# Kernel optimization log

Measured on AMD Instinct MI355X. Metric: run time of the kernel, lower is better.

## Reference

```python
import jax, jax.numpy as jnp
import numpy as np

B, N1, N2, D, H = 2, 1024, 1024, 2048, 16
DH = D // H  # 128


def _rope_tables(S, d):
    inv = 1.0 / (10000.0 ** (np.arange(0, d, 2, dtype=np.float32) / d))
    ang = np.outer(np.arange(S, dtype=np.float32), inv)  # [S, d/2]
    cos = np.repeat(np.cos(ang), 2, axis=-1).astype(np.float32)  # [S, d] interleaved pairs
    sin = np.repeat(np.sin(ang), 2, axis=-1).astype(np.float32)
    return jnp.asarray(cos), jnp.asarray(sin)


def setup_inputs() -> dict:
    key = jax.random.key(0)
    ks = jax.random.split(key, 24)
    sc = 0.02
    cos1, sin1 = _rope_tables(N1, DH)
    cos2, sin2 = _rope_tables(N2, DH)
    inp = {
        'x_1': jax.random.normal(ks[0], (B, N1, D), dtype=jnp.float32),
        'x_2': jax.random.normal(ks[1], (B, N2, D), dtype=jnp.float32),
        'cos1': cos1, 'sin1': sin1, 'cos2': cos2, 'sin2': sin2,
    }
    names = ['wq1', 'wk1', 'wv1', 'wo1', 'wq2', 'wk2', 'wv2', 'wo2']
    for i, n in enumerate(names):
        inp[n] = jax.random.normal(ks[2 + i], (D, D), dtype=jnp.float32) * sc
        inp['b' + n[1:]] = jax.random.normal(ks[10 + i], (D,), dtype=jnp.float32) * sc
    return inp


def _apply_rope(x, cos, sin):
    # x: [B, H, S, DH]; interleaved-pair rotation (use_real_unbind_dim=-1)
    xr = x.reshape(*x.shape[:-1], -1, 2)
    x_real, x_imag = xr[..., 0], xr[..., 1]
    x_rot = jnp.stack([-x_imag, x_real], axis=-1).reshape(x.shape)
    return x * cos[None, None] + x_rot * sin[None, None]


def _split_heads(t):
    b, n, _ = t.shape
    return t.reshape(b, n, H, DH).transpose(0, 2, 1, 3)  # b h n c


def reference(x_1, x_2, cos1, sin1, cos2, sin2,
              wq1, bq1, wk1, bk1, wv1, bv1, wo1, bo1,
              wq2, bq2, wk2, bk2, wv2, bv2, wo2, bo2):
    len_1 = x_1.shape[1]
    q = jnp.concatenate([x_1 @ wq1 + bq1, x_2 @ wq2 + bq2], axis=1)
    k = jnp.concatenate([x_1 @ wk1 + bk1, x_2 @ wk2 + bk2], axis=1)
    v = jnp.concatenate([x_1 @ wv1 + bv1, x_2 @ wv2 + bv2], axis=1)
    q, k, v = _split_heads(q), _split_heads(k), _split_heads(v)
    q = q * (DH ** -0.5)
    # per-position RoPE on the concatenated stream == per-stream RoPE then concat
    cos = jnp.concatenate([cos1, cos2], axis=0)
    sin = jnp.concatenate([sin1, sin2], axis=0)
    q = _apply_rope(q, cos, sin)
    k = _apply_rope(k, cos, sin)
    # joint attention over both streams (independent/cross_only flags = False)
    scores = jnp.einsum('bhqd,bhkd->bhqk', q, k)
    attn = jax.nn.softmax(scores, axis=-1)
    o = jnp.einsum('bhqk,bhkd->bhqd', attn, v)
    o = o.transpose(0, 2, 1, 3).reshape(o.shape[0], -1, H * DH)  # b n (h c)
    o1 = o[:, :len_1] @ wo1 + bo1
    o2 = o[:, len_1:] @ wo2 + bo2
    return (o1, o2)
```

## Files before the change

### kernel.cpp

```cpp
#include <hip/hip_runtime.h>
#include <hip/hip_bf16.h>

typedef __attribute__((ext_vector_type(4))) float f32x4;
typedef __attribute__((ext_vector_type(8))) short short8;
typedef __attribute__((ext_vector_type(4))) unsigned short us4;
typedef __attribute__((ext_vector_type(2))) unsigned short us2;
typedef unsigned short u16;

__device__ __forceinline__ float bf2f(u16 u) {
  unsigned int x = ((unsigned int)u) << 16;
  float f; __builtin_memcpy(&f, &x, 4); return f;
}
__device__ __forceinline__ u16 f2bf(float f) {
  __hip_bfloat16 h = __float2bfloat16(f);
  u16 u; __builtin_memcpy(&u, &h, 2); return u;
}

#define GLL16(g, l) __builtin_amdgcn_global_load_lds( \
    (const __attribute__((address_space(1))) unsigned int*)(g), \
    (__attribute__((address_space(3))) unsigned int*)(l), 16, 0, 0)

#define MFMA16x32(a, b, c) __builtin_amdgcn_mfma_f32_16x16x32_bf16(a, b, c, 0, 0, 0)


__global__ __launch_bounds__(256) void k_convert_x(const float* __restrict__ x1,
                                                   const float* __restrict__ x2,
                                                   u16* __restrict__ xc) {
  int tid = blockIdx.x * 256 + threadIdx.x;
  int e = tid * 8;
  int m = e >> 11, d = e & 2047;
  int b = m >> 11, n = m & 2047;
  const float* src = (n < 1024) ? (x1 + ((b << 10) + n) * 2048 + d)
                                : (x2 + ((b << 10) + n - 1024) * 2048 + d);
  float4 v0 = *(const float4*)src;
  float4 v1 = *(const float4*)(src + 4);
  us4 a = {f2bf(v0.x), f2bf(v0.y), f2bf(v0.z), f2bf(v0.w)};
  us4 c = {f2bf(v1.x), f2bf(v1.y), f2bf(v1.z), f2bf(v1.w)};
  *(us4*)(xc + e) = a;
  *(us4*)(xc + e + 4) = c;
}

struct W8 { const float* w[8]; };

__global__ __launch_bounds__(256) void k_wt(W8 p, u16* __restrict__ wtbase) {
  __shared__ u16 lt[64][72];
  const float* W = p.w[blockIdx.z];
  u16* Wt = wtbase + (size_t)blockIdx.z * 4194304u;
  int k0 = blockIdx.x * 64, n0 = blockIdx.y * 64;
  int t = threadIdx.x;
#pragma unroll
  for (int i = 0; i < 4; ++i) {
    int lin = t + i * 256;
    int r = lin >> 4, c4 = (lin & 15) * 4;
    float4 v = *(const float4*)&W[(k0 + r) * 2048 + n0 + c4];
    us4 u = {f2bf(v.x), f2bf(v.y), f2bf(v.z), f2bf(v.w)};
    *(us4*)&lt[r][c4] = u;
  }
  __syncthreads();
#pragma unroll
  for (int i = 0; i < 8; ++i) {
    int lin = t + i * 256;
    int rd = lin >> 5, cs = (lin & 31) * 2;
    us2 u = {lt[cs][rd], lt[cs + 1][rd]};
    *(us2*)&Wt[(n0 + rd) * 2048 + k0 + cs] = u;
  }
}

__global__ __launch_bounds__(256) void k_vt(const u16* __restrict__ V, u16* __restrict__ Vt) {
  __shared__ u16 lt[64][72];
  int b = blockIdx.z;
  int s0 = blockIdx.x * 64, d0 = blockIdx.y * 64;
  int t = threadIdx.x;
#pragma unroll
  for (int i = 0; i < 2; ++i) {
    int lin = t + i * 256;
    int r = lin >> 3, c8 = (lin & 7) * 8;
    short8 v = *(const short8*)&V[(b * 2048 + s0 + r) * 2048 + d0 + c8];
    *(short8*)&lt[r][c8] = v;
  }
  __syncthreads();
#pragma unroll
  for (int i = 0; i < 8; ++i) {
    int lin = t + i * 256;
    int rd = lin >> 5, cs = (lin & 31) * 2;
    us2 u = {lt[cs][rd], lt[cs + 1][rd]};
    *(us2*)&Vt[(b * 2048 + d0 + rd) * 2048 + s0 + cs] = u;
  }
}

__global__ __launch_bounds__(256) void k_rope(u16* __restrict__ Qb, u16* __restrict__ Kb,
                                              const float* __restrict__ cos1,
                                              const float* __restrict__ sin1,
                                              const float* __restrict__ cos2,
                                              const float* __restrict__ sin2) {
  u16* T = blockIdx.y ? Kb : Qb;
  const float scale = blockIdx.y ? 1.f : 0.08838834764831843f;
  int tid = blockIdx.x * 256 + threadIdx.x;
  int e = tid * 8;
  int m = e >> 11;
  int n = m & 2047;
  int dh0 = e & 127;
  const float* cr; const float* sr;
  if (n < 1024) { cr = cos1 + n * 128; sr = sin1 + n * 128; }
  else          { cr = cos2 + (n - 1024) * 128; sr = sin2 + (n - 1024) * 128; }
  float4 c0 = *(const float4*)(cr + dh0), c1 = *(const float4*)(cr + dh0 + 4);
  float4 s0 = *(const float4*)(sr + dh0), s1 = *(const float4*)(sr + dh0 + 4);
  short8 xv = *(short8*)(T + e);
  float x0 = bf2f((u16)xv[0]), x1 = bf2f((u16)xv[1]), x2 = bf2f((u16)xv[2]), x3 = bf2f((u16)xv[3]);
  float x4 = bf2f((u16)xv[4]), x5 = bf2f((u16)xv[5]), x6 = bf2f((u16)xv[6]), x7 = bf2f((u16)xv[7]);
  us4 o0 = { f2bf((x0 * c0.x - x1 * s0.x) * scale), f2bf((x1 * c0.x + x0 * s0.x) * scale),
             f2bf((x2 * c0.z - x3 * s0.z) * scale), f2bf((x3 * c0.z + x2 * s0.z) * scale) };
  us4 o1 = { f2bf((x4 * c1.x - x5 * s1.x) * scale), f2bf((x5 * c1.x + x4 * s1.x) * scale),
             f2bf((x6 * c1.z - x7 * s1.z) * scale), f2bf((x7 * c1.z + x6 * s1.z) * scale) };
  *(us4*)(T + e) = o0;
  *(us4*)(T + e + 4) = o1;
}

__device__ __forceinline__ void gemm256_core(const u16* __restrict__ A,
                                             const u16* __restrict__ Bt,
                                             int m0, int nb,
                                             u16* lA, u16* lB,
                                             f32x4 acc[8][4]) {
  const int t = threadIdx.x;
  const int lane = t & 63, wid = t >> 6;
  const int lq = lane & 15, lg = lane >> 4;
  const int wr = wid >> 2, wc = wid & 3;
  const int swz = (lq & 7) << 4;

  u16* lA0 = lA;  u16* lA1 = lA + 256 * 64;
  u16* lB0 = lB;  u16* lB1 = lB + 256 * 64;

  short8 af[4][2];
  short8 bf[2][2][2];

  auto stage = [&](const u16* G, int grow0, u16* lbase, int h, int kt) {
    const int k0 = (kt & 31) * 64;
#pragma unroll
    for (int j = 0; j < 2; ++j) {
      int c = j * 512 + t;
      int row = c >> 3;
      int colb = (c & 7) * 16;
      int sc = colb ^ ((row & 7) << 4);
      GLL16(G + (size_t)(grow0 + h * 128 + row) * 2048 + k0 + (sc >> 1),
            (u16*)((char*)lbase + (h * 128 + row) * 128 + colb));
    }
  };
  auto rdA = [&](const u16* lbase, int mh) {
#pragma unroll
    for (int mf = 0; mf < 4; ++mf)
#pragma unroll
      for (int kc = 0; kc < 2; ++kc) {
        int row = wr * 128 + (mh * 4 + mf) * 16 + lq;
        af[mf][kc] = *(const short8*)((const char*)lbase + row * 128 +
                                      ((kc * 64 + lg * 16) ^ swz));
      }
  };
  auto rdB = [&](const u16* lbase, int nh) {
#pragma unroll
    for (int nf = 0; nf < 2; ++nf)
#pragma unroll
      for (int kc = 0; kc < 2; ++kc) {
        int row = wc * 64 + (nh * 2 + nf) * 16 + lq;
        bf[nh][nf][kc] = *(const short8*)((const char*)lbase + row * 128 +
                                          ((kc * 64 + lg * 16) ^ swz));
      }
  };
  auto mm = [&](int mh, int nh) {
    __builtin_amdgcn_s_setprio(1);
#pragma unroll
    for (int mf = 0; mf < 4; ++mf)
#pragma unroll
      for (int nf = 0; nf < 2; ++nf)
#pragma unroll
        for (int kc = 0; kc < 2; ++kc)
          acc[mh * 4 + mf][nh * 2 + nf] =
              MFMA16x32(af[mf][kc], bf[nh][nf][kc], acc[mh * 4 + mf][nh * 2 + nf]);
    __builtin_amdgcn_s_setprio(0);
    __builtin_amdgcn_sched_barrier(0);
  };

#define LGK0() do { asm volatile("s_waitcnt lgkmcnt(0)" ::: "memory"); \
                    __builtin_amdgcn_sched_barrier(0); } while (0)
#define BAR()  __builtin_amdgcn_s_barrier()
#define VM4()  asm volatile("s_waitcnt vmcnt(4)" ::: "memory")

  stage(Bt, nb, lB0, 0, 0);
  stage(A,  m0, lA0, 0, 0);
  stage(Bt, nb, lB0, 1, 0);
  stage(A,  m0, lA0, 1, 0);
  stage(Bt, nb, lB1, 0, 1);
  stage(A,  m0, lA1, 0, 1);
  VM4();
  BAR();

#pragma unroll 1
  for (int i = 0; i < 16; ++i) {
    const int o1 = 2 * i + 1, e2 = 2 * i + 2, o3 = 2 * i + 3;
    rdA(lA0, 0); rdB(lB0, 0);
    stage(Bt, nb, lB1, 1, o1);
    BAR(); LGK0(); mm(0, 0); BAR();
    rdB(lB0, 1);
    stage(A, m0, lA1, 1, o1);
    BAR(); LGK0(); mm(0, 1); BAR();
    rdA(lA0, 1);
    stage(Bt, nb, lB0, 0, e2);
    BAR(); LGK0(); mm(1, 0); BAR();
    stage(A, m0, lA0, 0, e2);
    BAR(); LGK0(); mm(1, 1);
    VM4(); BAR();
    rdA(lA1, 0); rdB(lB1, 0);
    stage(Bt, nb, lB0, 1, e2);
    BAR(); LGK0(); mm(0, 0); BAR();
    rdB(lB1, 1);
    stage(A, m0, lA0, 1, e2);
    BAR(); LGK0(); mm(0, 1); BAR();
    rdA(lA1, 1);
    stage(Bt, nb, lB1, 0, o3);
    BAR(); LGK0(); mm(1, 0); BAR();
    stage(A, m0, lA1, 0, o3);
    BAR(); LGK0(); mm(1, 1);
    VM4(); BAR();
  }
#undef LGK0
#undef BAR
#undef VM4
}

struct QKV8P {
  const u16* wt[6];
  const float* bias[6];
  u16* out[3];
  const u16* xc;
};

__global__ __launch_bounds__(512, 2) void k_gemm_qkv(QKV8P p) {
  __shared__ __align__(16) u16 lA[2 * 256 * 64];
  __shared__ __align__(16) u16 lB[2 * 256 * 64];
  const int id = blockIdx.x;
  const int xcd = id & 7, sub = id >> 3;
  const int nt = xcd * 3 + (sub >> 4);
  const int mt = sub & 15;
  const int m0 = mt * 256;
  const int type = nt >> 3;
  const int colw = (nt & 7) * 256;
  const int strm = (mt >> 2) & 1;
  const int widx = type * 2 + strm;
  f32x4 acc[8][4];
  const f32x4 z4 = {0.f, 0.f, 0.f, 0.f};
#pragma unroll
  for (int a = 0; a < 8; ++a)
#pragma unroll
    for (int b = 0; b < 4; ++b) acc[a][b] = z4;
  gemm256_core(p.xc, p.wt[widx], m0, colw, lA, lB, acc);
  const int lane = threadIdx.x & 63, wid = threadIdx.x >> 6;
  const int lq = lane & 15, lg = lane >> 4;
  const int wr = wid >> 2, wc = wid & 3;
  u16* out = p.out[type];
  const float* bias = p.bias[widx];
#pragma unroll
  for (int nf = 0; nf < 4; ++nf) {
    int col = colw + wc * 64 + nf * 16 + lq;
    float bv = bias[col];
#pragma unroll
    for (int mf = 0; mf < 8; ++mf) {
      int row0 = m0 + wr * 128 + mf * 16 + lg * 4;
#pragma unroll
      for (int j = 0; j < 4; ++j)
        out[(size_t)(row0 + j) * 2048 + col] = f2bf(acc[mf][nf][j] + bv);
    }
  }
}

__global__ __launch_bounds__(512, 2) void k_gemm_out(const u16* __restrict__ O,
                                                     const u16* __restrict__ wt0,
                                                     const u16* __restrict__ wt1,
                                                     const float* __restrict__ b0,
                                                     const float* __restrict__ b1,
                                                     float* __restrict__ out) {
  __shared__ __align__(16) u16 lA[2 * 256 * 64];
  __shared__ __align__(16) u16 lB[2 * 256 * 64];
  const int id = blockIdx.x;
  const int nt = id & 7, mt = id >> 3;
  const int m0 = mt * 256;
  const int strm = (mt >> 2) & 1;
  f32x4 acc[8][4];
  const f32x4 z4 = {0.f, 0.f, 0.f, 0.f};
#pragma unroll
  for (int a = 0; a < 8; ++a)
#pragma unroll
    for (int b = 0; b < 4; ++b) acc[a][b] = z4;
  gemm256_core(O, strm ? wt1 : wt0, m0, nt * 256, lA, lB, acc);
  const float* bias = strm ? b1 : b0;
  float* obase = strm ? out + 4194304 : out;
  const int lane = threadIdx.x & 63, wid = threadIdx.x >> 6;
  const int lq = lane & 15, lg = lane >> 4;
  const int wr = wid >> 2, wc = wid & 3;
#pragma unroll
  for (int nf = 0; nf < 4; ++nf) {
    int col = nt * 256 + wc * 64 + nf * 16 + lq;
    float bv = bias[col];
#pragma unroll
    for (int mf = 0; mf < 8; ++mf) {
      int row0 = m0 + wr * 128 + mf * 16 + lg * 4;
#pragma unroll
      for (int j = 0; j < 4; ++j) {
        int row = row0 + j;
        int b = row >> 11, n = row & 2047;
        obase[(size_t)(b * 1024 + n - strm * 1024) * 2048 + col] = acc[mf][nf][j] + bv;
      }
    }
  }
}

__global__ __launch_bounds__(256) void k_attn(const u16* __restrict__ Q,
                                              const u16* __restrict__ K,
                                              const u16* __restrict__ Vt,
                                              u16* __restrict__ O) {
  __shared__ __align__(16) u16 kbuf[2][64 * 128];
  __shared__ __align__(16) u16 vbuf[2][128 * 64];
  __shared__ __align__(16) u16 pbuf[4][16 * 88];
  const int t = threadIdx.x, lane = t & 63, w = t >> 6;
  const int lq = lane & 15, g = lane >> 4;
  const int id = blockIdx.x;
  const int lgid = (id & 7) * 64 + (id >> 3);
  const int bh = lgid >> 4, qt = lgid & 15;
  const int b = bh >> 4, h = bh & 15;

  short8 qf[2][4];
#pragma unroll
  for (int u = 0; u < 2; ++u) {
    const u16* Qp = Q + (size_t)(b * 2048 + qt * 128 + w * 32 + u * 16 + lq) * 2048
                    + h * 128 + g * 8;
#pragma unroll
    for (int c = 0; c < 4; ++c) qf[u][c] = *(const short8*)(Qp + c * 32);
  }

  f32x4 oacc[2][8];
  const f32x4 z4 = {0.f, 0.f, 0.f, 0.f};
#pragma unroll
  for (int u = 0; u < 2; ++u)
#pragma unroll
    for (int dc = 0; dc < 8; ++dc) oacc[u][dc] = z4;
  float m_run[2] = {-1e30f, -1e30f}, l_run[2] = {0.f, 0.f};

  const int swz = (lq & 7) << 4;

  auto STAGE = [&](int bs, int kt) {
#pragma unroll
    for (int ii = 0; ii < 4; ++ii) {
      int i = w * 4 + ii;
      int o = i * 1024 + lane * 16;
      {
        int row = o >> 8, colb = o & 255;
        int sc = colb ^ ((row & 7) << 4);
        GLL16(K + (size_t)(b * 2048 + kt + row) * 2048 + h * 128 + (sc >> 1),
              (u16*)((char*)kbuf[bs] + o));
      }
      {
        int row = o >> 7, colb = o & 127;
        int sc = colb ^ ((row & 7) << 4);
        GLL16(Vt + (size_t)(b * 2048 + h * 128 + row) * 2048 + kt + (sc >> 1),
              (u16*)((char*)vbuf[bs] + o));
      }
    }
  };

  STAGE(0, 0);
  asm volatile("s_waitcnt vmcnt(0)" ::: "memory");
  __syncthreads();

  for (int tt = 0; tt < 32; ++tt) {
    const int cb = tt & 1;
    if (tt < 31) STAGE(cb ^ 1, (tt + 1) * 64);

    const char* kb = (const char*)kbuf[cb];
    const char* vb = (const char*)vbuf[cb];
    f32x4 s[2][4];
#pragma unroll
    for (int u = 0; u < 2; ++u)
#pragma unroll
      for (int kg = 0; kg < 4; ++kg) s[u][kg] = z4;
#pragma unroll
    for (int c = 0; c < 4; ++c) {
#pragma unroll
      for (int kg = 0; kg < 4; ++kg) {
        short8 kf = *(const short8*)(kb + (kg * 16 + lq) * 256 + ((c * 64 + g * 16) ^ swz));
        s[0][kg] = MFMA16x32(kf, qf[0][c], s[0][kg]);
        s[1][kg] = MFMA16x32(kf, qf[1][c], s[1][kg]);
      }
    }
    u16* pw = pbuf[w];
    short8 pb[2][2];
#pragma unroll
    for (int u = 0; u < 2; ++u) {
      float pm = -1e30f;
#pragma unroll
      for (int kg = 0; kg < 4; ++kg)
#pragma unroll
        for (int j = 0; j < 4; ++j) pm = fmaxf(pm, s[u][kg][j]);
      pm = fmaxf(pm, __shfl_xor(pm, 16));
      pm = fmaxf(pm, __shfl_xor(pm, 32));
      const float mnew = fmaxf(m_run[u], pm);
      const float r = __expf(m_run[u] - mnew);
      m_run[u] = mnew;
      float ps = 0.f;
#pragma unroll
      for (int kg = 0; kg < 4; ++kg) {
        float p0 = __expf(s[u][kg][0] - mnew), p1 = __expf(s[u][kg][1] - mnew);
        float p2 = __expf(s[u][kg][2] - mnew), p3 = __expf(s[u][kg][3] - mnew);
        ps += (p0 + p1) + (p2 + p3);
        us4 wv = {f2bf(p0), f2bf(p1), f2bf(p2), f2bf(p3)};
        *(us4*)(pw + lq * 88 + kg * 16 + g * 4) = wv;
      }
      ps += __shfl_xor(ps, 16);
      ps += __shfl_xor(ps, 32);
      l_run[u] = l_run[u] * r + ps;
#pragma unroll
      for (int dc = 0; dc < 8; ++dc) oacc[u][dc] = oacc[u][dc] * r;
      pb[u][0] = *(const short8*)(pw + lq * 88 + g * 8);
      pb[u][1] = *(const short8*)(pw + lq * 88 + 32 + g * 8);
    }
#pragma unroll
    for (int kc = 0; kc < 2; ++kc) {
#pragma unroll
      for (int dc = 0; dc < 8; ++dc) {
        short8 vf = *(const short8*)(vb + (dc * 16 + lq) * 128 + ((kc * 64 + g * 16) ^ swz));
        oacc[0][dc] = MFMA16x32(vf, pb[0][kc], oacc[0][dc]);
        oacc[1][dc] = MFMA16x32(vf, pb[1][kc], oacc[1][dc]);
      }
    }
    asm volatile("s_waitcnt vmcnt(0)" ::: "memory");
    __syncthreads();
  }

#pragma unroll
  for (int u = 0; u < 2; ++u) {
    const float inv = 1.f / l_run[u];
    u16* Op = O + (size_t)(b * 2048 + qt * 128 + w * 32 + u * 16 + lq) * 2048
              + h * 128 + g * 4;
#pragma unroll
    for (int dc = 0; dc < 8; ++dc) {
      us4 ov = {f2bf(oacc[u][dc][0] * inv), f2bf(oacc[u][dc][1] * inv),
                f2bf(oacc[u][dc][2] * inv), f2bf(oacc[u][dc][3] * inv)};
      *(us4*)(Op + dc * 16) = ov;
    }
  }
}


extern "C" void kernel_launch(void* const* d_in, const int* in_sizes, int n_in,
                              void* d_out, int out_size, void* d_ws, size_t ws_size,
                              hipStream_t stream) {
  const float* x1   = (const float*)d_in[0];
  const float* x2   = (const float*)d_in[1];
  const float* cos1 = (const float*)d_in[2];
  const float* sin1 = (const float*)d_in[3];
  const float* cos2 = (const float*)d_in[4];
  const float* sin2 = (const float*)d_in[5];
  W8 wp; const float* bias[8];
  for (int i = 0; i < 8; ++i) {
    wp.w[i] = (const float*)d_in[6 + 2 * i];
    bias[i] = (const float*)d_in[7 + 2 * i];
  }
  float* out = (float*)d_out;
  u16* ws = (u16*)d_ws;
  const size_t NX = 8388608;
  const size_t WSZ = 4194304;
  u16* xc = ws;
  u16* wt = ws + NX;
  u16* Qb = wt + 8 * WSZ;
  u16* Kb = Qb + NX;
  u16* Vb = Kb + NX;
  u16* Ob = Vb + NX;
  u16* Vt = xc;
  if (ws_size < (size_t)((Ob + NX) - ws) * sizeof(u16)) return;

  k_convert_x<<<dim3(4096), dim3(256), 0, stream>>>(x1, x2, xc);
  k_wt<<<dim3(32, 32, 8), dim3(256), 0, stream>>>(wp, wt);

  QKV8P qp;
  qp.wt[0] = wt + 0 * WSZ; qp.wt[1] = wt + 4 * WSZ;
  qp.wt[2] = wt + 1 * WSZ; qp.wt[3] = wt + 5 * WSZ;
  qp.wt[4] = wt + 2 * WSZ; qp.wt[5] = wt + 6 * WSZ;
  qp.bias[0] = bias[0]; qp.bias[1] = bias[4];
  qp.bias[2] = bias[1]; qp.bias[3] = bias[5];
  qp.bias[4] = bias[2]; qp.bias[5] = bias[6];
  qp.out[0] = Qb; qp.out[1] = Kb; qp.out[2] = Vb;
  qp.xc = xc;
  k_gemm_qkv<<<dim3(384), dim3(512), 0, stream>>>(qp);

  k_rope<<<dim3(4096, 2), dim3(256), 0, stream>>>(Qb, Kb, cos1, sin1, cos2, sin2);
  k_vt<<<dim3(32, 32, 2), dim3(256), 0, stream>>>(Vb, Vt);
  k_attn<<<dim3(512), dim3(256), 0, stream>>>(Qb, Kb, Vt, Ob);
  k_gemm_out<<<dim3(128), dim3(512), 0, stream>>>(Ob, wt + 3 * WSZ, wt + 7 * WSZ,
                                                  bias[3], bias[7], out);
}
```

Measured before the change: 387.9 us.

## Fuse RoPE into QKV GEMM epilogue and retile output projection GEMM

Removes the separate RoPE kernel by applying rotation and query scaling in the QKV GEMM epilogue, using a lane shuffle to fetch the paired element. Replaces the 256x256 pipelined output-projection GEMM with a simple 128x128 single-buffered kernel launched on a 32x16 grid for more blocks. Adds setprio around MFMA sections in attention and extra scheduling barriers in the GEMM core. The new output GEMM has no load/compute overlap, and the epilogue now does per-element cos/sin gathers.

```diff
diff --git a/kernel.cpp b/kernel.cpp
--- a/kernel.cpp
+++ b/kernel.cpp
@@ -88,33 +88,10 @@
   }
 }
 
-__global__ __launch_bounds__(256) void k_rope(u16* __restrict__ Qb, u16* __restrict__ Kb,
-                                              const float* __restrict__ cos1,
-                                              const float* __restrict__ sin1,
-                                              const float* __restrict__ cos2,
-                                              const float* __restrict__ sin2) {
-  u16* T = blockIdx.y ? Kb : Qb;
-  const float scale = blockIdx.y ? 1.f : 0.08838834764831843f;
-  int tid = blockIdx.x * 256 + threadIdx.x;
-  int e = tid * 8;
-  int m = e >> 11;
-  int n = m & 2047;
-  int dh0 = e & 127;
-  const float* cr; const float* sr;
-  if (n < 1024) { cr = cos1 + n * 128; sr = sin1 + n * 128; }
-  else          { cr = cos2 + (n - 1024) * 128; sr = sin2 + (n - 1024) * 128; }
-  float4 c0 = *(const float4*)(cr + dh0), c1 = *(const float4*)(cr + dh0 + 4);
-  float4 s0 = *(const float4*)(sr + dh0), s1 = *(const float4*)(sr + dh0 + 4);
-  short8 xv = *(short8*)(T + e);
-  float x0 = bf2f((u16)xv[0]), x1 = bf2f((u16)xv[1]), x2 = bf2f((u16)xv[2]), x3 = bf2f((u16)xv[3]);
-  float x4 = bf2f((u16)xv[4]), x5 = bf2f((u16)xv[5]), x6 = bf2f((u16)xv[6]), x7 = bf2f((u16)xv[7]);
-  us4 o0 = { f2bf((x0 * c0.x - x1 * s0.x) * scale), f2bf((x1 * c0.x + x0 * s0.x) * scale),
-             f2bf((x2 * c0.z - x3 * s0.z) * scale), f2bf((x3 * c0.z + x2 * s0.z) * scale) };
-  us4 o1 = { f2bf((x4 * c1.x - x5 * s1.x) * scale), f2bf((x5 * c1.x + x4 * s1.x) * scale),
-             f2bf((x6 * c1.z - x7 * s1.z) * scale), f2bf((x7 * c1.z + x6 * s1.z) * scale) };
-  *(us4*)(T + e) = o0;
-  *(us4*)(T + e + 4) = o1;
-}
+#define SB()  __builtin_amdgcn_sched_barrier(0)
+#define BAR() __builtin_amdgcn_s_barrier()
+#define VM4() asm volatile("s_waitcnt vmcnt(4)" ::: "memory")
+#define LGK0() do { asm volatile("s_waitcnt lgkmcnt(0)" ::: "memory"); SB(); } while (0)
 
 __device__ __forceinline__ void gemm256_core(const u16* __restrict__ A,
                                              const u16* __restrict__ Bt,
@@ -176,20 +153,12 @@
           acc[mh * 4 + mf][nh * 2 + nf] =
               MFMA16x32(af[mf][kc], bf[nh][nf][kc], acc[mh * 4 + mf][nh * 2 + nf]);
     __builtin_amdgcn_s_setprio(0);
-    __builtin_amdgcn_sched_barrier(0);
+    SB();
   };
 
-#define LGK0() do { asm volatile("s_waitcnt lgkmcnt(0)" ::: "memory"); \
-                    __builtin_amdgcn_sched_barrier(0); } while (0)
-#define BAR()  __builtin_amdgcn_s_barrier()
-#define VM4()  asm volatile("s_waitcnt vmcnt(4)" ::: "memory")
-
-  stage(Bt, nb, lB0, 0, 0);
-  stage(A,  m0, lA0, 0, 0);
-  stage(Bt, nb, lB0, 1, 0);
-  stage(A,  m0, lA0, 1, 0);
-  stage(Bt, nb, lB1, 0, 1);
-  stage(A,  m0, lA1, 0, 1);
+  stage(Bt, nb, lB0, 0, 0); stage(A, m0, lA0, 0, 0);
+  stage(Bt, nb, lB0, 1, 0); stage(A, m0, lA0, 1, 0);
+  stage(Bt, nb, lB1, 0, 1); stage(A, m0, lA1, 0, 1);
   VM4();
   BAR();
 
@@ -198,32 +167,30 @@
     const int o1 = 2 * i + 1, e2 = 2 * i + 2, o3 = 2 * i + 3;
     rdA(lA0, 0); rdB(lB0, 0);
     stage(Bt, nb, lB1, 1, o1);
-    BAR(); LGK0(); mm(0, 0); BAR();
+    SB(); BAR(); LGK0(); mm(0, 0); BAR();
     rdB(lB0, 1);
     stage(A, m0, lA1, 1, o1);
-    BAR(); LGK0(); mm(0, 1); BAR();
+    SB(); BAR(); LGK0(); mm(0, 1); BAR();
     rdA(lA0, 1);
     stage(Bt, nb, lB0, 0, e2);
-    BAR(); LGK0(); mm(1, 0); BAR();
+    SB(); BAR(); LGK0(); mm(1, 0); BAR();
     stage(A, m0, lA0, 0, e2);
-    BAR(); LGK0(); mm(1, 1);
+    SB(); BAR(); LGK0(); mm(1, 1);
     VM4(); BAR();
     rdA(lA1, 0); rdB(lB1, 0);
     stage(Bt, nb, lB0, 1, e2);
-    BAR(); LGK0(); mm(0, 0); BAR();
+    SB(); BAR(); LGK0(); mm(0, 0); BAR();
     rdB(lB1, 1);
     stage(A, m0, lA0, 1, e2);
-    BAR(); LGK0(); mm(0, 1); BAR();
+    SB(); BAR(); LGK0(); mm(0, 1); BAR();
     rdA(lA1, 1);
     stage(Bt, nb, lB1, 0, o3);
-    BAR(); LGK0(); mm(1, 0); BAR();
+    SB(); BAR(); LGK0(); mm(1, 0); BAR();
     stage(A, m0, lA1, 0, o3);
-    BAR(); LGK0(); mm(1, 1);
+    SB(); BAR(); LGK0(); mm(1, 1);
     VM4(); BAR();
   }
-#undef LGK0
-#undef BAR
-#undef VM4
+  asm volatile("s_waitcnt vmcnt(0) lgkmcnt(0)" ::: "memory");
 }
 
 struct QKV8P {
@@ -231,6 +198,7 @@
   const float* bias[6];
   u16* out[3];
   const u16* xc;
+  const float* cs[4];
 };
 
 __global__ __launch_bounds__(512, 2) void k_gemm_qkv(QKV8P p) {
@@ -252,61 +220,117 @@
 #pragma unroll
     for (int b = 0; b < 4; ++b) acc[a][b] = z4;
   gemm256_core(p.xc, p.wt[widx], m0, colw, lA, lB, acc);
+
   const int lane = threadIdx.x & 63, wid = threadIdx.x >> 6;
   const int lq = lane & 15, lg = lane >> 4;
   const int wr = wid >> 2, wc = wid & 3;
   u16* out = p.out[type];
   const float* bias = p.bias[widx];
+  const bool qk = (type < 2);
+  const float scale = (type == 0) ? 0.08838834764831843f : 1.f;
+  const float* c1 = p.cs[0]; const float* s1 = p.cs[1];
+  const float* c2 = p.cs[2]; const float* s2 = p.cs[3];
 #pragma unroll
   for (int nf = 0; nf < 4; ++nf) {
     int col = colw + wc * 64 + nf * 16 + lq;
     float bv = bias[col];
+    int dh = col & 127;
+    float sgn = (col & 1) ? 1.f : -1.f;
 #pragma unroll
     for (int mf = 0; mf < 8; ++mf) {
       int row0 = m0 + wr * 128 + mf * 16 + lg * 4;
 #pragma unroll
-      for (int j = 0; j < 4; ++j)
-        out[(size_t)(row0 + j) * 2048 + col] = f2bf(acc[mf][nf][j] + bv);
-    }
-  }
-}
-
-__global__ __launch_bounds__(512, 2) void k_gemm_out(const u16* __restrict__ O,
-                                                     const u16* __restrict__ wt0,
-                                                     const u16* __restrict__ wt1,
-                                                     const float* __restrict__ b0,
-                                                     const float* __restrict__ b1,
-                                                     float* __restrict__ out) {
-  __shared__ __align__(16) u16 lA[2 * 256 * 64];
-  __shared__ __align__(16) u16 lB[2 * 256 * 64];
-  const int id = blockIdx.x;
-  const int nt = id & 7, mt = id >> 3;
-  const int m0 = mt * 256;
-  const int strm = (mt >> 2) & 1;
-  f32x4 acc[8][4];
+      for (int j = 0; j < 4; ++j) {
+        int row = row0 + j;
+        float v = acc[mf][nf][j] + bv;
+        if (qk) {
+          float pv = __shfl_xor(v, 1);
+          int n = row & 2047;
+          const float* ct; const float* st; int nn;
+          if (n < 1024) { ct = c1; st = s1; nn = n; }
+          else          { ct = c2; st = s2; nn = n - 1024; }
+          float c = ct[nn * 128 + dh], s = st[nn * 128 + dh];
+          v = (v * c + sgn * pv * s) * scale;
+        }
+        out[(size_t)row * 2048 + col] = f2bf(v);
+      }
+    }
+  }
+}
+
+__device__ __forceinline__ void gemm128_core(const u16* __restrict__ A,
+                                             const u16* __restrict__ Bt,
+                                             u16* lA, u16* lB,
+                                             f32x4 acc[4][4], int m0, int n0) {
+  const int t = threadIdx.x;
+  const int lane = t & 63;
+  const int lq = lane & 15, lg = lane >> 4;
+  const int wr = (t >> 7) & 1, wc = (t >> 6) & 1;
+  for (int k0 = 0; k0 < 2048; k0 += 64) {
+    __syncthreads();
+#pragma unroll
+    for (int i = 0; i < 4; ++i) {
+      int chunk = i * 256 + t;
+      int r = chunk >> 3, c = chunk & 7;
+      GLL16(A + ((m0 + r) * 2048 + k0 + c * 8), lA + chunk * 8);
+      GLL16(Bt + ((n0 + r) * 2048 + k0 + c * 8), lB + chunk * 8);
+    }
+    asm volatile("s_waitcnt vmcnt(0)" ::: "memory");
+    __syncthreads();
+#pragma unroll
+    for (int kc = 0; kc < 2; ++kc) {
+      short8 af[4], bf[4];
+#pragma unroll
+      for (int rf = 0; rf < 4; ++rf)
+        af[rf] = *(const short8*)(lA + (wr * 64 + rf * 16 + lq) * 64 + kc * 32 + lg * 8);
+#pragma unroll
+      for (int cf = 0; cf < 4; ++cf)
+        bf[cf] = *(const short8*)(lB + (wc * 64 + cf * 16 + lq) * 64 + kc * 32 + lg * 8);
+      __builtin_amdgcn_s_setprio(1);
+#pragma unroll
+      for (int rf = 0; rf < 4; ++rf)
+#pragma unroll
+        for (int cf = 0; cf < 4; ++cf)
+          acc[rf][cf] = MFMA16x32(af[rf], bf[cf], acc[rf][cf]);
+      __builtin_amdgcn_s_setprio(0);
+    }
+  }
+}
+
+__global__ __launch_bounds__(256) void k_gemm_out(const u16* __restrict__ O,
+                                                  const u16* __restrict__ wt0,
+                                                  const u16* __restrict__ wt1,
+                                                  const float* __restrict__ b0,
+                                                  const float* __restrict__ b1,
+                                                  float* __restrict__ out) {
+  __shared__ u16 lA[128 * 64];
+  __shared__ u16 lB[128 * 64];
+  const int m0 = blockIdx.x * 128, n0 = blockIdx.y * 128;
+  const int stream1 = (m0 >> 10) & 1;
+  f32x4 acc[4][4];
   const f32x4 z4 = {0.f, 0.f, 0.f, 0.f};
 #pragma unroll
-  for (int a = 0; a < 8; ++a)
+  for (int a = 0; a < 4; ++a)
 #pragma unroll
     for (int b = 0; b < 4; ++b) acc[a][b] = z4;
-  gemm256_core(O, strm ? wt1 : wt0, m0, nt * 256, lA, lB, acc);
-  const float* bias = strm ? b1 : b0;
-  float* obase = strm ? out + 4194304 : out;
-  const int lane = threadIdx.x & 63, wid = threadIdx.x >> 6;
-  const int lq = lane & 15, lg = lane >> 4;
-  const int wr = wid >> 2, wc = wid & 3;
-#pragma unroll
-  for (int nf = 0; nf < 4; ++nf) {
-    int col = nt * 256 + wc * 64 + nf * 16 + lq;
+  gemm128_core(O, stream1 ? wt1 : wt0, lA, lB, acc, m0, n0);
+  const float* bias = stream1 ? b1 : b0;
+  const int lane = threadIdx.x & 63, lq = lane & 15, lg = lane >> 4;
+  const int wr = (threadIdx.x >> 7) & 1, wc = (threadIdx.x >> 6) & 1;
+#pragma unroll
+  for (int cf = 0; cf < 4; ++cf) {
+    int col = n0 + wc * 64 + cf * 16 + lq;
     float bv = bias[col];
 #pragma unroll
-    for (int mf = 0; mf < 8; ++mf) {
-      int row0 = m0 + wr * 128 + mf * 16 + lg * 4;
+    for (int rf = 0; rf < 4; ++rf) {
+      int row0 = m0 + wr * 64 + rf * 16 + lg * 4;
 #pragma unroll
       for (int j = 0; j < 4; ++j) {
         int row = row0 + j;
         int b = row >> 11, n = row & 2047;
-        obase[(size_t)(b * 1024 + n - strm * 1024) * 2048 + col] = acc[mf][nf][j] + bv;
+        float* dst = stream1 ? out + 4194304 + (((b << 10) + n - 1024) * 2048 + col)
+                             : out + (((b << 10) + n) * 2048 + col);
+        *dst = acc[rf][cf][j] + bv;
       }
     }
   }
@@ -380,6 +404,7 @@
     for (int u = 0; u < 2; ++u)
 #pragma unroll
       for (int kg = 0; kg < 4; ++kg) s[u][kg] = z4;
+    __builtin_amdgcn_s_setprio(1);
 #pragma unroll
     for (int c = 0; c < 4; ++c) {
 #pragma unroll
@@ -389,6 +414,7 @@
         s[1][kg] = MFMA16x32(kf, qf[1][c], s[1][kg]);
       }
     }
+    __builtin_amdgcn_s_setprio(0);
     u16* pw = pbuf[w];
     short8 pb[2][2];
 #pragma unroll
@@ -420,6 +446,7 @@
       pb[u][0] = *(const short8*)(pw + lq * 88 + g * 8);
       pb[u][1] = *(const short8*)(pw + lq * 88 + 32 + g * 8);
     }
+    __builtin_amdgcn_s_setprio(1);
 #pragma unroll
     for (int kc = 0; kc < 2; ++kc) {
 #pragma unroll
@@ -429,6 +456,7 @@
         oacc[1][dc] = MFMA16x32(vf, pb[1][kc], oacc[1][dc]);
       }
     }
+    __builtin_amdgcn_s_setprio(0);
     asm volatile("s_waitcnt vmcnt(0)" ::: "memory");
     __syncthreads();
   }
@@ -487,11 +515,11 @@
   qp.bias[4] = bias[2]; qp.bias[5] = bias[6];
   qp.out[0] = Qb; qp.out[1] = Kb; qp.out[2] = Vb;
   qp.xc = xc;
+  qp.cs[0] = cos1; qp.cs[1] = sin1; qp.cs[2] = cos2; qp.cs[3] = sin2;
   k_gemm_qkv<<<dim3(384), dim3(512), 0, stream>>>(qp);
 
-  k_rope<<<dim3(4096, 2), dim3(256), 0, stream>>>(Qb, Kb, cos1, sin1, cos2, sin2);
   k_vt<<<dim3(32, 32, 2), dim3(256), 0, stream>>>(Vb, Vt);
   k_attn<<<dim3(512), dim3(256), 0, stream>>>(Qb, Kb, Vt, Ob);
-  k_gemm_out<<<dim3(128), dim3(512), 0, stream>>>(Ob, wt + 3 * WSZ, wt + 7 * WSZ,
-                                                  bias[3], bias[7], out);
-}
+  k_gemm_out<<<dim3(32, 16), dim3(256), 0, stream>>>(Ob, wt + 3 * WSZ, wt + 7 * WSZ,
+                                                     bias[3], bias[7], out);
+}
```

New measurement: 467.2 us. 20.4% more time.
